# Kernel tuning notes

Measured on AMD Instinct MI355X. Metric: run time of the kernel, lower is better.

## Reference

```python
import jax, jax.numpy as jnp
import numpy as np
from jax import lax

K = 10
ALPHA = 0.1
N_NODES = 100000
N_EDGES = 3200000


def setup_inputs() -> dict:
    key = jax.random.key(0)
    ks = jax.random.split(key, 6)
    x = jax.random.normal(ks[0], (N_NODES, 256), dtype=jnp.float32)
    edge_index = jax.random.randint(ks[1], (2, N_EDGES), 0, N_NODES, dtype=jnp.int64)
    w1 = jax.random.normal(ks[2], (256, 256), dtype=jnp.float32) * (1.0 / np.sqrt(256))
    b1 = jax.random.normal(ks[3], (256,), dtype=jnp.float32) * 0.01
    w2 = jax.random.normal(ks[4], (64, 256), dtype=jnp.float32) * (1.0 / np.sqrt(256))
    b2 = jax.random.normal(ks[5], (64,), dtype=jnp.float32) * 0.01
    return {"x": x, "edge_index": edge_index, "w1": w1, "b1": b1, "w2": w2, "b2": b2}


def reference(x, edge_index, w1, b1, w2, b2):
    # Eval mode: dropout is identity.
    h = jax.nn.relu(x @ w1.T + b1)          # [N, hidden]
    z = h @ w2.T + b2                        # [N, out]

    n = x.shape[0]
    loop = jnp.arange(n, dtype=edge_index.dtype)
    row = jnp.concatenate([edge_index[0], loop])   # sources (with self-loops)
    col = jnp.concatenate([edge_index[1], loop])   # targets (with self-loops)

    # gcn_norm: D^{-1/2} (A + I) D^{-1/2}, degree at target nodes
    deg = jax.ops.segment_sum(jnp.ones_like(col, dtype=z.dtype), col, num_segments=n)
    dinv = lax.rsqrt(deg)                    # deg >= 1 due to self-loops
    norm = dinv[row] * dinv[col]             # [E+N]

    x0 = z

    def step(xk, _):
        msg = xk[row] * norm[:, None]                          # gather + scale
        agg = jax.ops.segment_sum(msg, col, num_segments=n)    # scatter-add
        return (1.0 - ALPHA) * agg + ALPHA * x0, None

    out, _ = lax.scan(step, z, None, length=K)
    return out
```

## Files before the change

kernel.cpp:

```cpp
#include <hip/hip_runtime.h>
#include <hip/hip_bf16.h>


#define HIDDEN 256
#define OUTF   64
#define NB_BLK 256

typedef __attribute__((ext_vector_type(8))) unsigned short ushort8;
typedef __attribute__((ext_vector_type(8))) short short8v;
typedef __attribute__((ext_vector_type(4))) float f32x4;

__device__ inline float b2f(unsigned short u) {
    union { unsigned int i; float f; } c;
    c.i = ((unsigned int)u) << 16;
    return c.f;
}
__device__ inline unsigned short f2b(float f) {
    union { float f; unsigned int i; } c;
    c.f = f;
    unsigned int x = c.i;
    unsigned int r = (x + 0x7fff + ((x >> 16) & 1)) >> 16;
    return (unsigned short)r;
}

__device__ inline bool detect_i64(const int* __restrict__ p) {
    int acc = 0;
#pragma unroll
    for (int i = 0; i < 16; ++i) acc |= p[2 * i + 1];
    return acc == 0;
}
__device__ inline int load_idx(const void* eiv, long long flat, bool is64) {
    if (is64) return (int)((const long long*)eiv)[flat];
    return ((const int*)eiv)[flat];
}

__global__ __launch_bounds__(256) void part_hist_kernel(const void* __restrict__ eiv,
                                                        long long E, int* __restrict__ bh,
                                                        int n, int nb) {
    __shared__ int hist[512];
    bool is64 = detect_i64((const int*)eiv);
    int t = threadIdx.x, b = blockIdx.x;
    for (int i = t; i < 512; i += 256) hist[i] = 0;
    __syncthreads();
    long long chunk = (E + NB_BLK - 1) / NB_BLK;
    long long beg = (long long)b * chunk, end = min(E, beg + chunk);
    for (long long e = beg + t; e < end; e += 256) {
        int c = load_idx(eiv, E + e, is64);
        if ((unsigned)c < (unsigned)n) atomicAdd(&hist[c >> 8], 1);
    }
    __syncthreads();
    for (int i = t; i < nb; i += 256) bh[i * NB_BLK + b] = hist[i];
}

__global__ __launch_bounds__(256) void part_colscan_kernel(const int* __restrict__ bh,
                                                           int* __restrict__ pre,
                                                           int* __restrict__ btot) {
    __shared__ int s[NB_BLK];
    int g = blockIdx.x, t = threadIdx.x;
    int v = bh[g * NB_BLK + t];
    s[t] = v;
    __syncthreads();
    for (int o = 1; o < NB_BLK; o <<= 1) {
        int tv = (t >= o) ? s[t - o] : 0;
        __syncthreads();
        s[t] += tv;
        __syncthreads();
    }
    pre[g * NB_BLK + t] = s[t] - v;
    if (t == NB_BLK - 1) btot[g] = s[t];
}

__global__ __launch_bounds__(512) void part_bscan_kernel(const int* __restrict__ btot,
                                                         int* __restrict__ bofs, int nb) {
    __shared__ int s[512];
    int t = threadIdx.x;
    int v = (t < nb) ? btot[t] : 0;
    s[t] = v;
    __syncthreads();
    for (int o = 1; o < 512; o <<= 1) {
        int tv = (t >= o) ? s[t - o] : 0;
        __syncthreads();
        s[t] += tv;
        __syncthreads();
    }
    if (t < nb) bofs[t] = s[t] - v;
    if (t == 511) bofs[nb] = s[511];
}

__global__ __launch_bounds__(256) void part_scatter_kernel(const void* __restrict__ eiv,
                                                           long long E,
                                                           const int* __restrict__ bofs,
                                                           const int* __restrict__ pre,
                                                           int2* __restrict__ pairs,
                                                           int n, int nb) {
    __shared__ int cur[512];
    bool is64 = detect_i64((const int*)eiv);
    int t = threadIdx.x, b = blockIdx.x;
    for (int i = t; i < nb; i += 256) cur[i] = bofs[i] + pre[i * NB_BLK + b];
    __syncthreads();
    long long chunk = (E + NB_BLK - 1) / NB_BLK;
    long long beg = (long long)b * chunk, end = min(E, beg + chunk);
    for (long long e = beg + t; e < end; e += 256) {
        int r = load_idx(eiv, e, is64);
        int c = load_idx(eiv, E + e, is64);
        if ((unsigned)c >= (unsigned)n || (unsigned)r >= (unsigned)n) continue;
        int pos = atomicAdd(&cur[c >> 8], 1);
        pairs[pos] = make_int2(c, r);
    }
}

__global__ __launch_bounds__(256) void csr_bucket_kernel(const int2* __restrict__ pairs,
                                                         const int* __restrict__ bofs,
                                                         int* __restrict__ ofs,
                                                         float* __restrict__ dinv,
                                                         int* __restrict__ csr_src,
                                                         int n, int nb) {
    __shared__ int hist[256];
    __shared__ int scn[256];
    int b = blockIdx.x;
    int t = threadIdx.x;
    int node0 = b << 8;
    int cnt = min(256, n - node0);

    hist[t] = 0;
    __syncthreads();
    int beg = bofs[b], end = bofs[b + 1];
    for (int e = beg + t; e < end; e += 256) atomicAdd(&hist[pairs[e].x & 255], 1);
    __syncthreads();
    int v = hist[t];
    scn[t] = v;
    __syncthreads();
    for (int o = 1; o < 256; o <<= 1) {
        int tv = (t >= o) ? scn[t - o] : 0;
        __syncthreads();
        scn[t] += tv;
        __syncthreads();
    }
    int excl = scn[t] - v;
    if (t < cnt) {
        ofs[node0 + t] = beg + excl;
        dinv[node0 + t] = rsqrtf((float)(v + 1));
    }
    if (b == nb - 1 && t == 0) ofs[n] = end;
    __syncthreads();
    hist[t] = beg + excl;
    __syncthreads();
    for (int e = beg + t; e < end; e += 256) {
        int2 p = pairs[e];
        int pos = atomicAdd(&hist[p.x & 255], 1);
        csr_src[pos] = p.y;
    }
}

#define MLP_BM 64
__global__ __launch_bounds__(256) void mlp_mfma_kernel(const float* __restrict__ x,
                                                       const float* __restrict__ w1,
                                                       const float* __restrict__ b1,
                                                       const float* __restrict__ w2,
                                                       const float* __restrict__ b2,
                                                       const float* __restrict__ dinv,
                                                       unsigned short* __restrict__ xb0,
                                                       unsigned short* __restrict__ g0, int n) {
    __shared__ __align__(16) unsigned short regA[16384];
    __shared__ __align__(16) unsigned short h_lds[64 * 264];

    const int t = threadIdx.x;
    const int w = t >> 6;
    const int l = t & 63;
    const int c = l & 15, g = l >> 4;
    const int node0 = blockIdx.x * MLP_BM;

    f32x4 acc[4][4];
#pragma unroll
    for (int a = 0; a < 4; ++a)
#pragma unroll
        for (int b = 0; b < 4; ++b) acc[a][b] = (f32x4)0.f;

    for (int ks = 0; ks < 8; ++ks) {
        const int k0 = ks * 32;
        {
            int kg = t & 3, m = t >> 2;
            int node = node0 + m;
            float4 A = make_float4(0.f, 0.f, 0.f, 0.f), B = A;
            if (node < n) {
                const float4* xp = (const float4*)(x + (size_t)node * HIDDEN + k0 + kg * 8);
                A = xp[0];
                B = xp[1];
            }
            short8v o;
            o[0] = (short)f2b(A.x); o[1] = (short)f2b(A.y);
            o[2] = (short)f2b(A.z); o[3] = (short)f2b(A.w);
            o[4] = (short)f2b(B.x); o[5] = (short)f2b(B.y);
            o[6] = (short)f2b(B.z); o[7] = (short)f2b(B.w);
            *(short8v*)&regA[8192 + (((m >> 4) * 64 + kg * 16 + (m & 15)) << 3)] = o;
        }
#pragma unroll
        for (int p = 0; p < 4; ++p) {
            int kg = t & 3, f = p * 64 + (t >> 2);
            const float4* wp = (const float4*)(w1 + (size_t)f * HIDDEN + k0 + kg * 8);
            float4 A = wp[0], B = wp[1];
            short8v o;
            o[0] = (short)f2b(A.x); o[1] = (short)f2b(A.y);
            o[2] = (short)f2b(A.z); o[3] = (short)f2b(A.w);
            o[4] = (short)f2b(B.x); o[5] = (short)f2b(B.y);
            o[6] = (short)f2b(B.z); o[7] = (short)f2b(B.w);
            *(short8v*)&regA[(((f >> 4) * 64 + kg * 16 + (f & 15)) << 3)] = o;
        }
        __syncthreads();
        short8v af[4], bf[4];
#pragma unroll
        for (int mt = 0; mt < 4; ++mt)
            af[mt] = *(const short8v*)&regA[8192 + ((mt * 64 + l) << 3)];
#pragma unroll
        for (int nt = 0; nt < 4; ++nt)
            bf[nt] = *(const short8v*)&regA[(((w * 4 + nt) * 64 + l) << 3)];
#pragma unroll
        for (int mt = 0; mt < 4; ++mt)
#pragma unroll
            for (int nt = 0; nt < 4; ++nt)
                acc[mt][nt] =
                    __builtin_amdgcn_mfma_f32_16x16x32_bf16(af[mt], bf[nt], acc[mt][nt], 0, 0, 0);
        __syncthreads();
    }

#pragma unroll
    for (int nt = 0; nt < 4; ++nt) {
        int col = w * 64 + nt * 16 + c;
        float b1v = b1[col];
#pragma unroll
        for (int mt = 0; mt < 4; ++mt)
#pragma unroll
            for (int r = 0; r < 4; ++r) {
                int row = mt * 16 + g * 4 + r;
                float hv = fmaxf(acc[mt][nt][r] + b1v, 0.f);
                h_lds[row * 264 + col] = f2b(hv);
            }
    }
#pragma unroll
    for (int p = 0; p < 8; ++p) {
        int j = p * 8 + (t >> 5);
        int kslot = t & 31;
        const float4* wp = (const float4*)(w2 + (size_t)j * HIDDEN + kslot * 8);
        float4 A = wp[0], B = wp[1];
        short8v o;
        o[0] = (short)f2b(A.x); o[1] = (short)f2b(A.y);
        o[2] = (short)f2b(A.z); o[3] = (short)f2b(A.w);
        o[4] = (short)f2b(B.x); o[5] = (short)f2b(B.y);
        o[6] = (short)f2b(B.z); o[7] = (short)f2b(B.w);
        *(short8v*)&regA[(((j >> 4) * 512 + (kslot >> 2) * 64 + (kslot & 3) * 16 + (j & 15)) << 3)] = o;
    }
    __syncthreads();

    f32x4 acc2[4];
#pragma unroll
    for (int nt = 0; nt < 4; ++nt) acc2[nt] = (f32x4)0.f;
#pragma unroll
    for (int ks = 0; ks < 8; ++ks) {
        short8v a2 = *(const short8v*)&h_lds[(w * 16 + c) * 264 + ks * 32 + g * 8];
#pragma unroll
        for (int nt = 0; nt < 4; ++nt) {
            short8v b2v = *(const short8v*)&regA[((nt * 512 + ks * 64 + l) << 3)];
            acc2[nt] = __builtin_amdgcn_mfma_f32_16x16x32_bf16(a2, b2v, acc2[nt], 0, 0, 0);
        }
    }
#pragma unroll
    for (int nt = 0; nt < 4; ++nt) {
        int col = nt * 16 + c;
        float bb = b2[col];
#pragma unroll
        for (int r = 0; r < 4; ++r) {
            int node = node0 + w * 16 + g * 4 + r;
            if (node < n) {
                float zv = acc2[nt][r] + bb;
                float di = dinv[node];
                xb0[(size_t)node * OUTF + col] = f2b(0.1f * zv);
                g0[(size_t)node * OUTF + col] = f2b(di * zv);
            }
        }
    }
}

template <int LAST>
__global__ __launch_bounds__(256) void prop_kernel(const unsigned short* __restrict__ gk,
                                                   const unsigned short* __restrict__ xb0,
                                                   unsigned short* __restrict__ gn,
                                                   float* __restrict__ out,
                                                   const int* __restrict__ ofs,
                                                   const int* __restrict__ csr_src,
                                                   const float* __restrict__ dinv, int n) {
    int gid = blockIdx.x * 256 + threadIdx.x;
    int node = gid >> 3;
    int part = gid & 7;
    if (node >= n) return;

    int beg = ofs[node];
    int end = ofs[node + 1];
    float di = dinv[node];

    float acc[8];
#pragma unroll
    for (int j = 0; j < 8; ++j) acc[j] = 0.f;

    const size_t poff = (size_t)part * 8;
    int e = beg;
    for (; e + 1 < end; e += 2) {
        int s0 = csr_src[e];
        int s1 = csr_src[e + 1];
        ushort8 a = *(const ushort8*)(gk + (size_t)s0 * OUTF + poff);
        ushort8 b = *(const ushort8*)(gk + (size_t)s1 * OUTF + poff);
#pragma unroll
        for (int j = 0; j < 8; ++j) acc[j] += b2f(a[j]);
#pragma unroll
        for (int j = 0; j < 8; ++j) acc[j] += b2f(b[j]);
    }
    if (e < end) {
        int s0 = csr_src[e];
        ushort8 a = *(const ushort8*)(gk + (size_t)s0 * OUTF + poff);
#pragma unroll
        for (int j = 0; j < 8; ++j) acc[j] += b2f(a[j]);
    }
    {
        ushort8 a = *(const ushort8*)(gk + (size_t)node * OUTF + poff);
#pragma unroll
        for (int j = 0; j < 8; ++j) acc[j] += b2f(a[j]);
    }

    ushort8 xv = *(const ushort8*)(xb0 + (size_t)node * OUTF + poff);
    float res[8];
#pragma unroll
    for (int j = 0; j < 8; ++j) res[j] = 0.9f * di * acc[j] + b2f(xv[j]);

    if (LAST) {
        float4* o4 = (float4*)(out + (size_t)node * OUTF + poff);
        o4[0] = make_float4(res[0], res[1], res[2], res[3]);
        o4[1] = make_float4(res[4], res[5], res[6], res[7]);
    } else {
        ushort8 o;
#pragma unroll
        for (int j = 0; j < 8; ++j) o[j] = f2b(di * res[j]);
        *(ushort8*)(gn + (size_t)node * OUTF + poff) = o;
    }
}

extern "C" void kernel_launch(void* const* d_in, const int* in_sizes, int n_in,
                              void* d_out, int out_size, void* d_ws, size_t ws_size,
                              hipStream_t stream) {
    const float* x = (const float*)d_in[0];
    const void* ei = d_in[1];
    const float* w1 = (const float*)d_in[2];
    const float* b1 = (const float*)d_in[3];
    const float* w2 = (const float*)d_in[4];
    const float* b2 = (const float*)d_in[5];
    float* out = (float*)d_out;

    int n = in_sizes[0] / HIDDEN;
    long long E = (long long)in_sizes[1] / 2;
    int nb = (n + 255) >> 8;

    char* ws = (char*)d_ws;
    size_t off = 0;
    auto alloc = [&](size_t bytes) {
        void* p = ws + off;
        off += (bytes + 511) & ~(size_t)511;
        return p;
    };
    unsigned short* xb0 = (unsigned short*)alloc((size_t)n * OUTF * 2);
    size_t gmark = off;
    unsigned short* gA = (unsigned short*)alloc((size_t)n * OUTF * 2);
    unsigned short* gB = (unsigned short*)alloc((size_t)n * OUTF * 2);
    int2* pairs = (int2*)(ws + gmark);
    float* dinv = (float*)alloc((size_t)n * 4);
    int* ofs = (int*)alloc((size_t)(n + 1) * 4);
    int* csr_src = (int*)alloc((size_t)E * 4);
    int* bh = (int*)alloc((size_t)512 * NB_BLK * 4);
    int* pre = (int*)alloc((size_t)512 * NB_BLK * 4);
    int* btot = (int*)alloc(512 * 4);
    int* bofs = (int*)alloc(513 * 4);

    part_hist_kernel<<<NB_BLK, 256, 0, stream>>>(ei, E, bh, n, nb);
    part_colscan_kernel<<<nb, NB_BLK, 0, stream>>>(bh, pre, btot);
    part_bscan_kernel<<<1, 512, 0, stream>>>(btot, bofs, nb);
    part_scatter_kernel<<<NB_BLK, 256, 0, stream>>>(ei, E, bofs, pre, pairs, n, nb);
    csr_bucket_kernel<<<nb, 256, 0, stream>>>(pairs, bofs, ofs, dinv, csr_src, n, nb);

    mlp_mfma_kernel<<<(n + MLP_BM - 1) / MLP_BM, 256, 0, stream>>>(x, w1, b1, w2, b2, dinv,
                                                                   xb0, gA, n);

    int prop_blocks = (int)(((size_t)n * 8 + 255) / 256);
    for (int k = 0; k < 10; ++k) {
        const unsigned short* gin = (k & 1) ? gB : gA;
        unsigned short* gout = (k & 1) ? gA : gB;
        if (k == 9) {
            prop_kernel<1><<<prop_blocks, 256, 0, stream>>>(gin, xb0, nullptr, out, ofs,
                                                            csr_src, dinv, n);
        } else {
            prop_kernel<0><<<prop_blocks, 256, 0, stream>>>(gin, xb0, gout, nullptr, ofs,
                                                            csr_src, dinv, n);
        }
    }
}
```

Baseline: 725.7 us.

## Split feature dim into two 32-wide slabs for propagation and prepack weights

Stores the propagated features and the scaled input as two separate 32-column bf16 slabs, and runs each propagation step as two launches over half the features. The per-slab gather working set (6.4MB per buffer) is meant to fit better in cache, cutting the cost of random neighbour reads. The MLP now uses weights prepacked to bf16 once by a new kernel, so each block no longer converts them, and it reads W2 directly from global memory. In exchange it doubles the prop launches and re-reads the CSR indices once per slab.

```diff
diff --git a/kernel.cpp b/kernel.cpp
--- a/kernel.cpp
+++ b/kernel.cpp
@@ -21,6 +21,16 @@
     unsigned int x = c.i;
     unsigned int r = (x + 0x7fff + ((x >> 16) & 1)) >> 16;
     return (unsigned short)r;
+}
+__device__ inline short8v cvt8(const float* s) {
+    float4 A = ((const float4*)s)[0];
+    float4 B = ((const float4*)s)[1];
+    short8v o;
+    o[0] = (short)f2b(A.x); o[1] = (short)f2b(A.y);
+    o[2] = (short)f2b(A.z); o[3] = (short)f2b(A.w);
+    o[4] = (short)f2b(B.x); o[5] = (short)f2b(B.y);
+    o[6] = (short)f2b(B.z); o[7] = (short)f2b(B.w);
+    return o;
 }
 
 __device__ inline bool detect_i64(const int* __restrict__ p) {
@@ -152,23 +162,44 @@
     }
 }
 
-#define MLP_BM 64
+__global__ __launch_bounds__(256) void pack_w_kernel(const float* __restrict__ w1,
+                                                     const float* __restrict__ w2,
+                                                     unsigned short* __restrict__ w1p,
+                                                     unsigned short* __restrict__ w2p) {
+    int id = blockIdx.x * 256 + threadIdx.x;
+    if (id < 8192) {
+        int ks = id >> 10, rem = id & 1023;
+        int f = rem >> 2, kg = rem & 3;
+        short8v o = cvt8(w1 + (size_t)f * HIDDEN + ks * 32 + kg * 8);
+        *(short8v*)(w1p + ((size_t)(ks * 1024 + (f >> 4) * 64 + kg * 16 + (f & 15)) << 3)) = o;
+    } else if (id < 8192 + 2048) {
+        int q = id - 8192;
+        int j = q >> 5, kslot = q & 31;
+        short8v o = cvt8(w2 + (size_t)j * HIDDEN + kslot * 8);
+        *(short8v*)(w2p +
+                    ((size_t)((j >> 4) * 512 + (kslot >> 2) * 64 + (kslot & 3) * 16 + (j & 15))
+                     << 3)) = o;
+    }
+}
+
 __global__ __launch_bounds__(256) void mlp_mfma_kernel(const float* __restrict__ x,
-                                                       const float* __restrict__ w1,
+                                                       const unsigned short* __restrict__ w1p,
                                                        const float* __restrict__ b1,
-                                                       const float* __restrict__ w2,
+                                                       const unsigned short* __restrict__ w2p,
                                                        const float* __restrict__ b2,
                                                        const float* __restrict__ dinv,
-                                                       unsigned short* __restrict__ xb0,
+                                                       unsigned short* __restrict__ xb,
                                                        unsigned short* __restrict__ g0, int n) {
-    __shared__ __align__(16) unsigned short regA[16384];
-    __shared__ __align__(16) unsigned short h_lds[64 * 264];
+    __shared__ __align__(16) union {
+        struct { unsigned short w1s[8192]; unsigned short xs[2048]; } p1;
+        unsigned short h[64 * 264];
+    } u;
 
     const int t = threadIdx.x;
     const int w = t >> 6;
     const int l = t & 63;
     const int c = l & 15, g = l >> 4;
-    const int node0 = blockIdx.x * MLP_BM;
+    const int node0 = blockIdx.x * 64;
 
     f32x4 acc[4][4];
 #pragma unroll
@@ -177,43 +208,29 @@
         for (int b = 0; b < 4; ++b) acc[a][b] = (f32x4)0.f;
 
     for (int ks = 0; ks < 8; ++ks) {
-        const int k0 = ks * 32;
         {
             int kg = t & 3, m = t >> 2;
             int node = node0 + m;
-            float4 A = make_float4(0.f, 0.f, 0.f, 0.f), B = A;
-            if (node < n) {
-                const float4* xp = (const float4*)(x + (size_t)node * HIDDEN + k0 + kg * 8);
-                A = xp[0];
-                B = xp[1];
+            short8v o = (short8v)0;
+            if (node < n) o = cvt8(x + (size_t)node * HIDDEN + ks * 32 + kg * 8);
+            *(short8v*)&u.p1.xs[((m >> 4) * 64 + kg * 16 + (m & 15)) << 3] = o;
+        }
+        {
+            const unsigned short* wsrc = w1p + (size_t)ks * 8192;
+#pragma unroll
+            for (int i = 0; i < 4; ++i) {
+                int unit = i * 256 + t;
+                *(short8v*)&u.p1.w1s[unit << 3] = *(const short8v*)(wsrc + ((size_t)unit << 3));
             }
-            short8v o;
-            o[0] = (short)f2b(A.x); o[1] = (short)f2b(A.y);
-            o[2] = (short)f2b(A.z); o[3] = (short)f2b(A.w);
-            o[4] = (short)f2b(B.x); o[5] = (short)f2b(B.y);
-            o[6] = (short)f2b(B.z); o[7] = (short)f2b(B.w);
-            *(short8v*)&regA[8192 + (((m >> 4) * 64 + kg * 16 + (m & 15)) << 3)] = o;
         }
-#pragma unroll
-        for (int p = 0; p < 4; ++p) {
-            int kg = t & 3, f = p * 64 + (t >> 2);
-            const float4* wp = (const float4*)(w1 + (size_t)f * HIDDEN + k0 + kg * 8);
-            float4 A = wp[0], B = wp[1];
-            short8v o;
-            o[0] = (short)f2b(A.x); o[1] = (short)f2b(A.y);
-            o[2] = (short)f2b(A.z); o[3] = (short)f2b(A.w);
-            o[4] = (short)f2b(B.x); o[5] = (short)f2b(B.y);
-            o[6] = (short)f2b(B.z); o[7] = (short)f2b(B.w);
-            *(short8v*)&regA[(((f >> 4) * 64 + kg * 16 + (f & 15)) << 3)] = o;
-        }
         __syncthreads();
         short8v af[4], bf[4];
 #pragma unroll
         for (int mt = 0; mt < 4; ++mt)
-            af[mt] = *(const short8v*)&regA[8192 + ((mt * 64 + l) << 3)];
+            af[mt] = *(const short8v*)&u.p1.xs[(mt * 64 + l) << 3];
 #pragma unroll
         for (int nt = 0; nt < 4; ++nt)
-            bf[nt] = *(const short8v*)&regA[(((w * 4 + nt) * 64 + l) << 3)];
+            bf[nt] = *(const short8v*)&u.p1.w1s[((w * 4 + nt) * 64 + l) << 3];
 #pragma unroll
         for (int mt = 0; mt < 4; ++mt)
 #pragma unroll
@@ -232,23 +249,9 @@
 #pragma unroll
             for (int r = 0; r < 4; ++r) {
                 int row = mt * 16 + g * 4 + r;
-                float hv = fmaxf(acc[mt][nt][r] + b1v, 0.f);
-                h_lds[row * 264 + col] = f2b(hv);
+                u.h[row * 264 + col] = f2b(fmaxf(acc[mt][nt][r] + b1v, 0.f));
             }
     }
-#pragma unroll
-    for (int p = 0; p < 8; ++p) {
-        int j = p * 8 + (t >> 5);
-        int kslot = t & 31;
-        const float4* wp = (const float4*)(w2 + (size_t)j * HIDDEN + kslot * 8);
-        float4 A = wp[0], B = wp[1];
-        short8v o;
-        o[0] = (short)f2b(A.x); o[1] = (short)f2b(A.y);
-        o[2] = (short)f2b(A.z); o[3] = (short)f2b(A.w);
-        o[4] = (short)f2b(B.x); o[5] = (short)f2b(B.y);
-        o[6] = (short)f2b(B.z); o[7] = (short)f2b(B.w);
-        *(short8v*)&regA[(((j >> 4) * 512 + (kslot >> 2) * 64 + (kslot & 3) * 16 + (j & 15)) << 3)] = o;
-    }
     __syncthreads();
 
     f32x4 acc2[4];
@@ -256,16 +259,18 @@
     for (int nt = 0; nt < 4; ++nt) acc2[nt] = (f32x4)0.f;
 #pragma unroll
     for (int ks = 0; ks < 8; ++ks) {
-        short8v a2 = *(const short8v*)&h_lds[(w * 16 + c) * 264 + ks * 32 + g * 8];
+        short8v a2 = *(const short8v*)&u.h[(w * 16 + c) * 264 + ks * 32 + g * 8];
 #pragma unroll
         for (int nt = 0; nt < 4; ++nt) {
-            short8v b2v = *(const short8v*)&regA[((nt * 512 + ks * 64 + l) << 3)];
-            acc2[nt] = __builtin_amdgcn_mfma_f32_16x16x32_bf16(a2, b2v, acc2[nt], 0, 0, 0);
+            short8v bv = *(const short8v*)(w2p + ((size_t)(nt * 512 + ks * 64 + l) << 3));
+            acc2[nt] = __builtin_amdgcn_mfma_f32_16x16x32_bf16(a2, bv, acc2[nt], 0, 0, 0);
         }
     }
 #pragma unroll
     for (int nt = 0; nt < 4; ++nt) {
         int col = nt * 16 + c;
+        int s = nt >> 1;
+        int col32 = (nt & 1) * 16 + c;
         float bb = b2[col];
 #pragma unroll
         for (int r = 0; r < 4; ++r) {
@@ -273,8 +278,9 @@
             if (node < n) {
                 float zv = acc2[nt][r] + bb;
                 float di = dinv[node];
-                xb0[(size_t)node * OUTF + col] = f2b(0.1f * zv);
-                g0[(size_t)node * OUTF + col] = f2b(di * zv);
+                size_t idx = (size_t)s * n * 32 + (size_t)node * 32 + col32;
+                xb[idx] = f2b(0.1f * zv);
+                g0[idx] = f2b(di * zv);
             }
         }
     }
@@ -282,15 +288,16 @@
 
 template <int LAST>
 __global__ __launch_bounds__(256) void prop_kernel(const unsigned short* __restrict__ gk,
-                                                   const unsigned short* __restrict__ xb0,
+                                                   const unsigned short* __restrict__ xbs,
                                                    unsigned short* __restrict__ gn,
                                                    float* __restrict__ out,
                                                    const int* __restrict__ ofs,
                                                    const int* __restrict__ csr_src,
-                                                   const float* __restrict__ dinv, int n) {
+                                                   const float* __restrict__ dinv,
+                                                   int n, int sbase) {
     int gid = blockIdx.x * 256 + threadIdx.x;
-    int node = gid >> 3;
-    int part = gid & 7;
+    int node = gid >> 2;
+    int part = gid & 3;
     if (node >= n) return;
 
     int beg = ofs[node];
@@ -306,8 +313,8 @@
     for (; e + 1 < end; e += 2) {
         int s0 = csr_src[e];
         int s1 = csr_src[e + 1];
-        ushort8 a = *(const ushort8*)(gk + (size_t)s0 * OUTF + poff);
-        ushort8 b = *(const ushort8*)(gk + (size_t)s1 * OUTF + poff);
+        ushort8 a = *(const ushort8*)(gk + ((size_t)s0 << 5) + poff);
+        ushort8 b = *(const ushort8*)(gk + ((size_t)s1 << 5) + poff);
 #pragma unroll
         for (int j = 0; j < 8; ++j) acc[j] += b2f(a[j]);
 #pragma unroll
@@ -315,30 +322,30 @@
     }
     if (e < end) {
         int s0 = csr_src[e];
-        ushort8 a = *(const ushort8*)(gk + (size_t)s0 * OUTF + poff);
+        ushort8 a = *(const ushort8*)(gk + ((size_t)s0 << 5) + poff);
 #pragma unroll
         for (int j = 0; j < 8; ++j) acc[j] += b2f(a[j]);
     }
     {
-        ushort8 a = *(const ushort8*)(gk + (size_t)node * OUTF + poff);
+        ushort8 a = *(const ushort8*)(gk + ((size_t)node << 5) + poff);
 #pragma unroll
         for (int j = 0; j < 8; ++j) acc[j] += b2f(a[j]);
     }
 
-    ushort8 xv = *(const ushort8*)(xb0 + (size_t)node * OUTF + poff);
+    ushort8 xv = *(const ushort8*)(xbs + ((size_t)node << 5) + poff);
     float res[8];
 #pragma unroll
     for (int j = 0; j < 8; ++j) res[j] = 0.9f * di * acc[j] + b2f(xv[j]);
 
     if (LAST) {
-        float4* o4 = (float4*)(out + (size_t)node * OUTF + poff);
+        float4* o4 = (float4*)(out + (size_t)node * OUTF + sbase + poff);
         o4[0] = make_float4(res[0], res[1], res[2], res[3]);
         o4[1] = make_float4(res[4], res[5], res[6], res[7]);
     } else {
         ushort8 o;
 #pragma unroll
         for (int j = 0; j < 8; ++j) o[j] = f2b(di * res[j]);
-        *(ushort8*)(gn + (size_t)node * OUTF + poff) = o;
+        *(ushort8*)(gn + ((size_t)node << 5) + poff) = o;
     }
 }
 
@@ -364,10 +371,10 @@
         off += (bytes + 511) & ~(size_t)511;
         return p;
     };
-    unsigned short* xb0 = (unsigned short*)alloc((size_t)n * OUTF * 2);
+    size_t N32 = (size_t)n * 32;
+    unsigned short* xb = (unsigned short*)alloc(2 * N32 * 2);
     size_t gmark = off;
-    unsigned short* gA = (unsigned short*)alloc((size_t)n * OUTF * 2);
-    unsigned short* gB = (unsigned short*)alloc((size_t)n * OUTF * 2);
+    unsigned short* gbuf = (unsigned short*)alloc(4 * N32 * 2);
     int2* pairs = (int2*)(ws + gmark);
     float* dinv = (float*)alloc((size_t)n * 4);
     int* ofs = (int*)alloc((size_t)(n + 1) * 4);
@@ -376,6 +383,10 @@
     int* pre = (int*)alloc((size_t)512 * NB_BLK * 4);
     int* btot = (int*)alloc(512 * 4);
     int* bofs = (int*)alloc(513 * 4);
+    unsigned short* w1p = (unsigned short*)alloc(65536 * 2);
+    unsigned short* w2p = (unsigned short*)alloc(16384 * 2);
+
+    pack_w_kernel<<<40, 256, 0, stream>>>(w1, w2, w1p, w2p);
 
     part_hist_kernel<<<NB_BLK, 256, 0, stream>>>(ei, E, bh, n, nb);
     part_colscan_kernel<<<nb, NB_BLK, 0, stream>>>(bh, pre, btot);
@@ -383,19 +394,22 @@
     part_scatter_kernel<<<NB_BLK, 256, 0, stream>>>(ei, E, bofs, pre, pairs, n, nb);
     csr_bucket_kernel<<<nb, 256, 0, stream>>>(pairs, bofs, ofs, dinv, csr_src, n, nb);
 
-    mlp_mfma_kernel<<<(n + MLP_BM - 1) / MLP_BM, 256, 0, stream>>>(x, w1, b1, w2, b2, dinv,
-                                                                   xb0, gA, n);
-
-    int prop_blocks = (int)(((size_t)n * 8 + 255) / 256);
+    mlp_mfma_kernel<<<(n + 63) / 64, 256, 0, stream>>>(x, w1p, b1, w2p, b2, dinv, xb, gbuf, n);
+
+    int prop_blocks = (int)(((size_t)n * 4 + 255) / 256);
     for (int k = 0; k < 10; ++k) {
-        const unsigned short* gin = (k & 1) ? gB : gA;
-        unsigned short* gout = (k & 1) ? gA : gB;
-        if (k == 9) {
-            prop_kernel<1><<<prop_blocks, 256, 0, stream>>>(gin, xb0, nullptr, out, ofs,
-                                                            csr_src, dinv, n);
-        } else {
-            prop_kernel<0><<<prop_blocks, 256, 0, stream>>>(gin, xb0, gout, nullptr, ofs,
-                                                            csr_src, dinv, n);
+        int ppi = k & 1, ppo = (k + 1) & 1;
+        for (int s = 0; s < 2; ++s) {
+            const unsigned short* gin = gbuf + ((size_t)(ppi * 2 + s)) * N32;
+            unsigned short* gout = gbuf + ((size_t)(ppo * 2 + s)) * N32;
+            const unsigned short* xbs = xb + (size_t)s * N32;
+            if (k == 9) {
+                prop_kernel<1><<<prop_blocks, 256, 0, stream>>>(gin, xbs, nullptr, out, ofs,
+                                                                csr_src, dinv, n, s * 32);
+            } else {
+                prop_kernel<0><<<prop_blocks, 256, 0, stream>>>(gin, xbs, gout, nullptr, ofs,
+                                                                csr_src, dinv, n, s * 32);
+            }
         }
     }
 }
```

After: 1.195 ms. 1.65x slower.
